# Performance work log

Measured on AMD Instinct MI355X. Metric: run time of the kernel, lower is better.

Reference implementation:

```python
import jax, jax.numpy as jnp
import numpy as np

BLOCK = 16
GROUPS = 16
HIDDEN = 512
SEQ = BLOCK * GROUPS  # 256
B = 512


def setup_inputs() -> dict:
    key = jax.random.key(0)
    kx, kw = jax.random.split(key)
    x = jax.random.normal(kx, (B, HIDDEN, 1, SEQ), dtype=jnp.float32)
    # Conv2d weight (PACKED, 16, 1, 1) reshaped to per-group 16x16 matrices:
    # W[h, out_ch, in_ch]. Torch default init ~ U(-1/sqrt(fan_in), 1/sqrt(fan_in)).
    bound = 1.0 / np.sqrt(BLOCK)
    W = jax.random.uniform(kw, (HIDDEN, BLOCK, BLOCK), dtype=jnp.float32,
                           minval=-bound, maxval=bound)
    return {"x": x, "W": W}


def reference(x, W):
    # x: (B, HIDDEN, 1, SEQ) -> (B, HIDDEN, BLOCK, GROUPS)
    Bsz = x.shape[0]
    x4 = x.reshape(Bsz, HIDDEN, BLOCK, GROUPS)
    # Grouped 1x1 conv with groups=HIDDEN, 16 channels/group == per-group
    # 16x16 matmul over the BLOCK axis, applied independently at each of the
    # GROUPS spatial positions: y[b,h,o,g] = sum_i W[h,o,i] * x[b,h,i,g]
    y4 = jnp.einsum('hoi,bhig->bhog', W, x4)
    return y4.reshape(Bsz, HIDDEN, 1, SEQ)
```

## Files before the change

kernel.cpp:

```cpp
#include <hip/hip_runtime.h>

typedef __attribute__((ext_vector_type(4))) float floatx4;

#define NH 512
#define NB 512
#define TILE 256
#define BPW 32

__global__ __launch_bounds__(256, 4) void GlobalMixer_kernel(
    const float* __restrict__ x,
    const float* __restrict__ w,
    float* __restrict__ y)
{
    const int lane = threadIdx.x & 63;
    const int wv   = threadIdx.x >> 6;
    const int gid  = blockIdx.x * 4 + wv;
    const int h    = gid & (NH - 1);
    const int b0   = (gid >> 9) * BPW;
    const int o    = lane >> 2;
    const int g0   = (lane & 3) * 4;

    const float* wrow_p = w + h * TILE + o * 16;
    float wr[16];
    #pragma unroll
    for (int i = 0; i < 4; ++i) {
        floatx4 wq = *(const floatx4*)(wrow_p + i * 4);
        wr[i * 4 + 0] = wq.x; wr[i * 4 + 1] = wq.y;
        wr[i * 4 + 2] = wq.z; wr[i * 4 + 3] = wq.w;
    }

    const size_t bstride = (size_t)NH * TILE;
    const size_t tile0   = ((size_t)b0 * NH + h) * TILE;
    const float* xp = x + tile0 + g0;
    float*       yp = y + tile0 + o * 16 + g0;

    for (int bi = 0; bi < BPW; ++bi) {
        floatx4 acc = {0.f, 0.f, 0.f, 0.f};
        #pragma unroll
        for (int i = 0; i < 16; ++i) {
            floatx4 xv = *(const floatx4*)(xp + i * 16);
            acc += wr[i] * xv;
        }
        *(floatx4*)yp = acc;

        xp += bstride;
        yp += bstride;
    }
}

extern "C" void kernel_launch(void* const* d_in, const int* in_sizes, int n_in,
                              void* d_out, int out_size, void* d_ws, size_t ws_size,
                              hipStream_t stream) {
    const float* x = (const float*)d_in[0];
    const float* w = (const float*)d_in[1];
    float*       y = (float*)d_out;

    dim3 grid(2048), block(256);
    hipLaunchKernelGGL(GlobalMixer_kernel, grid, block, 0, stream, x, w, y);
}
```

Baseline: 620.7 us.

## Stage x tiles through LDS with register prefetch and 4 outputs per lane

Each wave now loads four batch tiles with coalesced float4 loads, one per lane, writes them to LDS, and reads them back so every lane computes four output rows for one batch. Weights for four output channels are held in registers. The next group of tiles is prefetched into registers while the current group is computed. This replaces the strided redundant global reads of x with one coalesced load per element, in exchange for extra LDS traffic, higher register use and fewer waves per SIMD (launch bound lowered from 4 to 3).

```diff
diff --git a/kernel.cpp b/kernel.cpp
--- a/kernel.cpp
+++ b/kernel.cpp
@@ -6,46 +6,87 @@
 #define NB 512
 #define TILE 256
 #define BPW 32
+#define NGRP 8
+#define SLOTF 272
 
-__global__ __launch_bounds__(256, 4) void GlobalMixer_kernel(
+__global__ __launch_bounds__(256, 3) void GlobalMixer_kernel(
     const float* __restrict__ x,
     const float* __restrict__ w,
     float* __restrict__ y)
 {
+    __shared__ float lds[4][4][SLOTF];
+
     const int lane = threadIdx.x & 63;
     const int wv   = threadIdx.x >> 6;
     const int gid  = blockIdx.x * 4 + wv;
     const int h    = gid & (NH - 1);
     const int b0   = (gid >> 9) * BPW;
-    const int o    = lane >> 2;
-    const int g0   = (lane & 3) * 4;
+    const int t    = lane >> 4;
+    const int og   = (lane >> 2) & 3;
+    const int q    = lane & 3;
 
-    const float* wrow_p = w + h * TILE + o * 16;
-    float wr[16];
-    #pragma unroll
-    for (int i = 0; i < 4; ++i) {
-        floatx4 wq = *(const floatx4*)(wrow_p + i * 4);
-        wr[i * 4 + 0] = wq.x; wr[i * 4 + 1] = wq.y;
-        wr[i * 4 + 2] = wq.z; wr[i * 4 + 3] = wq.w;
+    float wreg[4][16];
+    {
+        const float* wp = w + h * TILE + (og * 4) * 16;
+        #pragma unroll
+        for (int j = 0; j < 4; ++j)
+            #pragma unroll
+            for (int i4 = 0; i4 < 4; ++i4) {
+                floatx4 wq = *(const floatx4*)(wp + j * 16 + i4 * 4);
+                wreg[j][i4 * 4 + 0] = wq.x; wreg[j][i4 * 4 + 1] = wq.y;
+                wreg[j][i4 * 4 + 2] = wq.z; wreg[j][i4 * 4 + 3] = wq.w;
+            }
     }
 
     const size_t bstride = (size_t)NH * TILE;
-    const size_t tile0   = ((size_t)b0 * NH + h) * TILE;
-    const float* xp = x + tile0 + g0;
-    float*       yp = y + tile0 + o * 16 + g0;
 
-    for (int bi = 0; bi < BPW; ++bi) {
-        floatx4 acc = {0.f, 0.f, 0.f, 0.f};
+    const float* xl = x + ((size_t)b0 * NH + h) * TILE + lane * 4;
+    float*       yg = y + ((size_t)(b0 + t) * NH + h) * TILE + og * 64 + q * 4;
+
+    float*       ldsw = &lds[wv][0][0];
+    const float* ldsr = &lds[wv][t][0];
+
+    floatx4 sA[4], sB[4];
+
+    #pragma unroll
+    for (int k = 0; k < 4; ++k)
+        sA[k] = *(const floatx4*)(xl + (size_t)k * bstride);
+
+    const float* xg = xl + 4 * bstride;
+
+    auto body = [&](floatx4* cur, floatx4* nxt, bool prefetch) {
+        if (prefetch) {
+            #pragma unroll
+            for (int k = 0; k < 4; ++k)
+                nxt[k] = *(const floatx4*)(xg + (size_t)k * bstride);
+            xg += 4 * bstride;
+        }
+        #pragma unroll
+        for (int k = 0; k < 4; ++k)
+            *(floatx4*)(ldsw + k * SLOTF + lane * 4) = cur[k];
+        floatx4 acc0 = {0.f,0.f,0.f,0.f}, acc1 = {0.f,0.f,0.f,0.f};
+        floatx4 acc2 = {0.f,0.f,0.f,0.f}, acc3 = {0.f,0.f,0.f,0.f};
         #pragma unroll
         for (int i = 0; i < 16; ++i) {
-            floatx4 xv = *(const floatx4*)(xp + i * 16);
-            acc += wr[i] * xv;
+            floatx4 xv = *(const floatx4*)(ldsr + i * 16 + q * 4);
+            acc0 += wreg[0][i] * xv;
+            acc1 += wreg[1][i] * xv;
+            acc2 += wreg[2][i] * xv;
+            acc3 += wreg[3][i] * xv;
         }
-        *(floatx4*)yp = acc;
+        *(floatx4*)(yg + 0 * 16) = acc0;
+        *(floatx4*)(yg + 1 * 16) = acc1;
+        *(floatx4*)(yg + 2 * 16) = acc2;
+        *(floatx4*)(yg + 3 * 16) = acc3;
+        yg += 4 * bstride;
+    };
 
-        xp += bstride;
-        yp += bstride;
+    for (int g = 0; g < NGRP - 2; g += 2) {
+        body(sA, sB, true);
+        body(sB, sA, true);
     }
+    body(sA, sB, true);
+    body(sB, sA, false);
 }
 
 extern "C" void kernel_launch(void* const* d_in, const int* in_sizes, int n_in,
```

Result: slower. 1.183 ms (+90.6%).
